# Kernel tuning notes

Hardware: AMD Instinct MI355X
Metric: run time of the kernel (lower is better)

## Reference

```python
import jax, jax.numpy as jnp
import numpy as np

N = 100000   # nodes
E = 1600000  # edges (avg degree 16)
IN = 24
HID = 128
OUT = 12


def setup_inputs() -> dict:
    key = jax.random.key(0)
    ks = jax.random.split(key, 16)
    s = 0.05
    return {
        "inputs": jax.random.normal(ks[0], (N, IN), jnp.float32),
        "src": jax.random.randint(ks[1], (E,), 0, N),
        "dst": jax.random.randint(ks[2], (E,), 0, N),
        "e_w": jax.random.uniform(ks[3], (E, 1), jnp.float32),
        "snorm_n": jax.random.uniform(ks[4], (N, 1), jnp.float32),
        "snorm_e": jax.random.uniform(ks[5], (E, 1), jnp.float32),
        "W_emb": jax.random.normal(ks[6], (IN, HID), jnp.float32) * s,
        "b_emb": jnp.zeros((HID,), jnp.float32),
        "W_self1": jax.random.normal(ks[7], (HID, HID), jnp.float32) * s,
        "W1": jax.random.normal(ks[8], (HID, HID), jnp.float32) * s,
        "b1": jnp.zeros((HID,), jnp.float32),
        "W_self2": jax.random.normal(ks[9], (HID, HID), jnp.float32) * s,
        "W2": jax.random.normal(ks[10], (HID, HID), jnp.float32) * s,
        "b2": jnp.zeros((HID,), jnp.float32),
        "W_fc": jax.random.normal(ks[11], (HID, OUT), jnp.float32) * s,
        "b_fc": jnp.zeros((OUT,), jnp.float32),
    }


def _degrees(src, dst):
    out_deg = jnp.clip(jnp.zeros((N,), jnp.float32).at[src].add(1.0), 1.0)
    in_deg = jnp.clip(jnp.zeros((N,), jnp.float32).at[dst].add(1.0), 1.0)
    return out_deg, in_deg


def _gcn_layer(h, src, dst, e_w, out_deg, in_deg, W_self, W, b):
    # self transform (no bias)
    h_s = h @ W_self
    # source-side symmetric norm, edge-weighted message, sum-aggregate at dst
    feat = h * (out_deg ** -0.5)[:, None]          # [N, H]
    m = feat[src] * e_w                            # [E, H]  u_mul_e
    agg = jax.ops.segment_sum(m, dst, num_segments=N)  # [N, H] sum reduce
    h2 = (agg @ W + b) * (in_deg ** -0.5)[:, None]
    return h_s + h2


def reference(inputs, src, dst, e_w, snorm_n, snorm_e,
              W_emb, b_emb, W_self1, W1, b1, W_self2, W2, b2, W_fc, b_fc):
    out_deg, in_deg = _degrees(src, dst)
    h = inputs @ W_emb + b_emb
    h = jax.nn.relu(_gcn_layer(h, src, dst, e_w, out_deg, in_deg, W_self1, W1, b1))
    h = jax.nn.relu(_gcn_layer(h, src, dst, e_w, out_deg, in_deg, W_self2, W2, b2))
    return h @ W_fc + b_fc
```

## Files before the change

### kernel.cpp

```cpp
#include <hip/hip_runtime.h>

#define NN 100000
#define EE 1600000
#define IN_F 24
#define HID 128
#define OUT_F 12
#define LBLK 128

#define NBKT 782
#define PA_BLKS 256
#define PA_EPB 6250

#define OW_BITS 13
#define OWIN 8192
#define OW_GRP 13
#define OW_CPY 48
#define OW_EPB 33334

#define RCAP 2560

#define EMB_B 2048
#define PREP_B 264
#define ONORM_B 196
#define K1_GRID (PA_BLKS + EMB_B + PREP_B + ONORM_B)

typedef unsigned char u8;
typedef unsigned short u16;
typedef unsigned int u32;
typedef unsigned long long u64;

using short8 = __attribute__((ext_vector_type(8))) short;
using f32x4  = __attribute__((ext_vector_type(4))) float;

__device__ __forceinline__ float bf2f(u16 h) {
  return __uint_as_float(((u32)h) << 16);
}
__device__ __forceinline__ u16 f2bf(float f) {
  u32 u = __float_as_uint(f);
  u32 r = (u + 0x7FFFu + ((u >> 16) & 1u)) >> 16;
  return (u16)r;
}
__device__ __forceinline__ float inv_sqrt_cnt(int c) {
  if (c < 1) c = 1;
  return 1.0f / sqrtf((float)c);
}

__global__ __launch_bounds__(256) void k_odeg(const int* __restrict__ src,
                                              u32* __restrict__ whist) {
  __shared__ u32 hist[OWIN / 2];
  int b = blockIdx.x, t = threadIdx.x;
  int g = b / OW_CPY, sb = b % OW_CPY;
  for (int i = t; i < OWIN / 2; i += 256) hist[i] = 0;
  __syncthreads();
  int e0 = sb * OW_EPB;
  int e1 = e0 + OW_EPB; if (e1 > EE) e1 = EE;
  for (int e = e0 + t; e < e1; e += 256) {
    int s = src[e];
    if ((s >> OW_BITS) == g) {
      int i = s & (OWIN - 1);
      atomicAdd(&hist[i >> 1], (i & 1) ? 0x10000u : 1u);
    }
  }
  __syncthreads();
  u32* out = whist + (size_t)b * (OWIN / 2);
  for (int i = t; i < OWIN / 2; i += 256) out[i] = hist[i];
}

__device__ __forceinline__ void emb_body(int eb, const float* __restrict__ inputs,
                                         const float* __restrict__ W_emb,
                                         const float* __restrict__ b_emb,
                                         u16* __restrict__ harr, float* smemW) {
  int t = threadIdx.x;
  float* Wls = smemW;
  float* bls = smemW + IN_F * HID;
  for (int i = t; i < IN_F * HID; i += 256) Wls[i] = W_emb[i];
  if (t < HID) bls[t] = b_emb[t];
  __syncthreads();
  int c = t & 127;
  int sub = t >> 7;
  for (int node = eb * 2 + sub; node < NN; node += EMB_B * 2) {
    const float* xr = inputs + (size_t)node * IN_F;
    float acc = bls[c];
    #pragma unroll
    for (int k = 0; k < IN_F; ++k) acc = fmaf(xr[k], Wls[k * HID + c], acc);
    harr[(size_t)node * HID + c] = f2bf(acc);
  }
}

__device__ __forceinline__ void prep_body(int pb,
    const float* __restrict__ Ws1, const float* __restrict__ W1m,
    const float* __restrict__ Ws2, const float* __restrict__ W2m,
    const float* __restrict__ Wfc,
    u16* __restrict__ WT1, u16* __restrict__ WT2, u16* __restrict__ WfcT) {
  int idx = pb * 256 + (int)threadIdx.x;
  if (idx < 65536) {
    int layer = idx >> 15;
    int rem = idx & 32767;
    int n = rem >> 8, k = rem & 255;
    const float* A = layer ? Ws2 : Ws1;
    const float* B = layer ? W2m : W1m;
    float v = (k < HID) ? A[(size_t)k * HID + n] : B[(size_t)(k - HID) * HID + n];
    (layer ? WT2 : WT1)[(size_t)n * 256 + k] = f2bf(v);
  } else if (idx < 65536 + 2048) {
    int j = idx - 65536;
    int n = j >> 7, k = j & 127;
    WfcT[(size_t)n * 128 + k] = f2bf(n < OUT_F ? Wfc[(size_t)k * OUT_F + n] : 0.f);
  }
}

__device__ __forceinline__ void onorm_body(int ob, const u32* __restrict__ whist,
                                           float* __restrict__ out_norm) {
  int i = ob * 256 + (int)threadIdx.x;
  if (i >= NN / 2) return;
  int n0 = 2 * i;
  int g = n0 >> OW_BITS;
  int pi = (n0 & (OWIN - 1)) >> 1;
  const u32* base = whist + (size_t)g * OW_CPY * (OWIN / 2) + pi;
  u32 s = 0;
  #pragma unroll 8
  for (int c = 0; c < OW_CPY; ++c) s += base[(size_t)c * (OWIN / 2)];
  out_norm[n0]     = inv_sqrt_cnt((int)(s & 0xFFFFu));
  out_norm[n0 + 1] = inv_sqrt_cnt((int)(s >> 16));
}

__global__ __launch_bounds__(256) void k1(
    const int* __restrict__ dst, u32* __restrict__ histgD,
    const float* __restrict__ inputs, const float* __restrict__ W_emb,
    const float* __restrict__ b_emb, u16* __restrict__ harr,
    const float* __restrict__ Ws1, const float* __restrict__ W1m,
    const float* __restrict__ Ws2, const float* __restrict__ W2m,
    const float* __restrict__ Wfc,
    u16* __restrict__ WT1, u16* __restrict__ WT2, u16* __restrict__ WfcT,
    const u32* __restrict__ whist, float* __restrict__ out_norm) {
  __shared__ __align__(16) char sm[13312];
  int b = blockIdx.x, t = threadIdx.x;
  if (b < PA_BLKS) {
    u32* histD = (u32*)sm;
    for (int i = t; i < 1024; i += 256) histD[i] = 0;
    __syncthreads();
    int e0 = b * PA_EPB;
    for (int e = e0 + t; e < e0 + PA_EPB; e += 256)
      atomicAdd(&histD[dst[e] >> 7], 1u);
    __syncthreads();
    for (int i = t; i < 1024; i += 256) histgD[(size_t)b * 1024 + i] = histD[i];
  } else if (b < PA_BLKS + EMB_B) {
    emb_body(b - PA_BLKS, inputs, W_emb, b_emb, harr, (float*)sm);
  } else if (b < PA_BLKS + EMB_B + PREP_B) {
    prep_body(b - PA_BLKS - EMB_B, Ws1, W1m, Ws2, W2m, Wfc, WT1, WT2, WfcT);
  } else {
    onorm_body(b - PA_BLKS - EMB_B - PREP_B, whist, out_norm);
  }
}

__global__ __launch_bounds__(256) void k_scan1(u32* __restrict__ histgD,
                                               u32* __restrict__ totalsD) {
  __shared__ u32 s[256];
  int k = blockIdx.x, t = threadIdx.x;
  u32 v = histgD[(size_t)t * 1024 + k];
  s[t] = v;
  __syncthreads();
  for (int off = 1; off < 256; off <<= 1) {
    u32 a = (t >= off) ? s[t - off] : 0;
    __syncthreads();
    s[t] += a;
    __syncthreads();
  }
  histgD[(size_t)t * 1024 + k] = s[t] - v;
  if (t == 255) totalsD[k] = s[255];
}

__global__ __launch_bounds__(1024) void k_scan2(const u32* __restrict__ totalsD,
                                                u32* __restrict__ estartD) {
  __shared__ u32 s[1024];
  int t = threadIdx.x;
  u32 v = (t < NBKT) ? totalsD[t] : 0;
  s[t] = v;
  __syncthreads();
  for (int off = 1; off < 1024; off <<= 1) {
    u32 a = (t >= off) ? s[t - off] : 0;
    __syncthreads();
    s[t] += a;
    __syncthreads();
  }
  if (t < NBKT) estartD[t] = s[t] - v;
  if (t == NBKT - 1) estartD[NBKT] = s[t];
}

__global__ __launch_bounds__(256) void k_passb(
    const int* __restrict__ src, const int* __restrict__ dst,
    const float* __restrict__ e_w,
    const u32* __restrict__ histgD, const u32* __restrict__ estartD,
    u64* __restrict__ ebuf) {
  __shared__ u32 cur[1024];
  int pb = blockIdx.x, t = threadIdx.x;
  for (int i = t; i < 1024; i += 256)
    cur[i] = ((i < NBKT) ? estartD[i] : 0u) + histgD[(size_t)pb * 1024 + i];
  __syncthreads();
  int e0 = pb * PA_EPB;
  for (int e = e0 + t; e < e0 + PA_EPB; e += 256) {
    int s = src[e], d = dst[e];
    u32 hi = (u32)s | (((u32)(d & 127)) << 17);
    u64 rec = ((u64)hi << 32) | (u64)__float_as_uint(e_w[e]);
    u32 pos = atomicAdd(&cur[d >> 7], 1u);
    ebuf[pos] = rec;
  }
}

__global__ __launch_bounds__(256) void k_reorder(
    u64* __restrict__ ebuf, const u32* __restrict__ estart,
    int* __restrict__ row_start, float* __restrict__ in_norm) {
  __shared__ u64 stage[RCAP];
  __shared__ u32 cnt[128], pfx[128], cur[128];
  int k = blockIdx.x, t = threadIdx.x;
  if (t < 128) cnt[t] = 0;
  __syncthreads();
  int e0 = (int)estart[k], e1 = (int)estart[k + 1];
  int n = e1 - e0; if (n > RCAP) n = RCAP;
  for (int i = t; i < n; i += 256) {
    u64 v = ebuf[e0 + i];
    stage[i] = v;
    atomicAdd(&cnt[(u32)(v >> 49) & 127], 1u);
  }
  __syncthreads();
  if (t < 128) pfx[t] = cnt[t];
  __syncthreads();
  for (int off = 1; off < 128; off <<= 1) {
    u32 v = (t < 128 && t >= off) ? pfx[t - off] : 0;
    __syncthreads();
    if (t < 128) pfx[t] += v;
    __syncthreads();
  }
  if (t < 128) {
    u32 start = (u32)e0 + pfx[t] - cnt[t];
    cur[t] = start;
    int node = k * 128 + t;
    if (node < NN) {
      row_start[node] = (int)start;
      in_norm[node] = inv_sqrt_cnt((int)cnt[t]);
    }
  }
  if (k == NBKT - 1 && t == 0) row_start[NN] = e1;
  __syncthreads();
  for (int i = t; i < n; i += 256) {
    u64 v = stage[i];
    u32 pos = atomicAdd(&cur[(u32)(v >> 49) & 127], 1u);
    ebuf[pos] = v;
  }
}

__global__ __launch_bounds__(256) void k_agg(const u16* __restrict__ harr,
                                             const int* __restrict__ row_start,
                                             const float* __restrict__ in_norm,
                                             const float* __restrict__ out_norm,
                                             const u64* __restrict__ ebuf,
                                             u16* __restrict__ aggr) {
  int t = threadIdx.x;
  int node = blockIdx.x * 8 + (t >> 5);
  if (node >= NN) return;
  int lane = t & 31;
  int s0 = row_start[node], s1 = row_start[node + 1];
  float ax = 0.f, ay = 0.f, az = 0.f, aw = 0.f;
  for (int i0 = s0; i0 < s1; i0 += 32) {
    u32 pk2 = 0;
    if (i0 + lane < s1) {
      u64 rec = ebuf[i0 + lane];
      u32 sv = (u32)(rec >> 32) & 0x1FFFF;
      float w = __uint_as_float((u32)rec) * out_norm[sv];
      pk2 = (((u32)f2bf(w)) << 17) | sv;
    }
    int m = s1 - i0; if (m > 32) m = 32;
    int j = 0;
    for (; j + 4 <= m; j += 4) {
      u32 p0 = __shfl(pk2, j,     32);
      u32 p1 = __shfl(pk2, j + 1, 32);
      u32 p2 = __shfl(pk2, j + 2, 32);
      u32 p3 = __shfl(pk2, j + 3, 32);
      ushort4 h0 = *(const ushort4*)(harr + (size_t)(p0 & 0x1FFFF) * HID + lane * 4);
      ushort4 h1 = *(const ushort4*)(harr + (size_t)(p1 & 0x1FFFF) * HID + lane * 4);
      ushort4 h2 = *(const ushort4*)(harr + (size_t)(p2 & 0x1FFFF) * HID + lane * 4);
      ushort4 h3 = *(const ushort4*)(harr + (size_t)(p3 & 0x1FFFF) * HID + lane * 4);
      float w0 = bf2f((u16)(p0 >> 17));
      float w1 = bf2f((u16)(p1 >> 17));
      float w2 = bf2f((u16)(p2 >> 17));
      float w3 = bf2f((u16)(p3 >> 17));
      ax = fmaf(w0, bf2f(h0.x), ax); ay = fmaf(w0, bf2f(h0.y), ay);
      az = fmaf(w0, bf2f(h0.z), az); aw = fmaf(w0, bf2f(h0.w), aw);
      ax = fmaf(w1, bf2f(h1.x), ax); ay = fmaf(w1, bf2f(h1.y), ay);
      az = fmaf(w1, bf2f(h1.z), az); aw = fmaf(w1, bf2f(h1.w), aw);
      ax = fmaf(w2, bf2f(h2.x), ax); ay = fmaf(w2, bf2f(h2.y), ay);
      az = fmaf(w2, bf2f(h2.z), az); aw = fmaf(w2, bf2f(h2.w), aw);
      ax = fmaf(w3, bf2f(h3.x), ax); ay = fmaf(w3, bf2f(h3.y), ay);
      az = fmaf(w3, bf2f(h3.z), az); aw = fmaf(w3, bf2f(h3.w), aw);
    }
    for (; j < m; ++j) {
      u32 p = __shfl(pk2, j, 32);
      float w = bf2f((u16)(p >> 17));
      ushort4 hv = *(const ushort4*)(harr + (size_t)(p & 0x1FFFF) * HID + lane * 4);
      ax = fmaf(w, bf2f(hv.x), ax); ay = fmaf(w, bf2f(hv.y), ay);
      az = fmaf(w, bf2f(hv.z), az); aw = fmaf(w, bf2f(hv.w), aw);
    }
  }
  float inn = in_norm[node];
  ushort4 r;
  r.x = f2bf(ax * inn); r.y = f2bf(ay * inn);
  r.z = f2bf(az * inn); r.w = f2bf(aw * inn);
  *(ushort4*)(aggr + (size_t)node * HID + lane * 4) = r;
}

template<int FC>
__global__ __launch_bounds__(512) void k_layer(u16* __restrict__ harr,
    const u16* __restrict__ aggr,
    const u16* __restrict__ WT, const float* __restrict__ bias,
    const float* __restrict__ in_norm,
    const u16* __restrict__ WfcT, const float* __restrict__ b_fc,
    float* __restrict__ out) {
  __shared__ char smem[135168];
  const int t = threadIdx.x;
  const int r0 = blockIdx.x * LBLK;

  #pragma unroll
  for (int i = 0; i < 4; ++i) {
    int boff = i * 8192 + t * 16;
    int row = boff >> 8, col = boff & 255;
    uint4 v = *(const uint4*)(harr + (size_t)(r0 + row) * HID + (col >> 1));
    *(uint4*)(smem + row * 512 + (col ^ ((row & 7) << 4))) = v;
  }
  #pragma unroll
  for (int i = 0; i < 4; ++i) {
    int boff = i * 8192 + t * 16;
    int row = boff >> 8, col = boff & 255;
    uint4 v = *(const uint4*)(aggr + (size_t)(r0 + row) * HID + (col >> 1));
    *(uint4*)(smem + row * 512 + (256 + (col ^ ((row & 7) << 4)))) = v;
  }
  #pragma unroll
  for (int i = 0; i < 8; ++i) {
    int boff = i * 8192 + t * 16;
    int row = boff >> 9, col = boff & 511;
    uint4 v = *(const uint4*)(WT + (size_t)row * 256 + (col >> 1));
    *(uint4*)(smem + 65536 + row * 512 + (col ^ ((row & 7) << 4))) = v;
  }
  if (FC && t < 256) {
    int row = t >> 4, col = (t & 15) * 16;
    uint4 v = *(const uint4*)(WfcT + (size_t)row * 128 + (col >> 1));
    *(uint4*)(smem + 131072 + row * 256 + (col ^ ((row & 7) << 4))) = v;
  }
  __syncthreads();

  const int lane = t & 63, w = t >> 6;
  const int l15 = lane & 15, lhi = lane >> 4;

  f32x4 acc[8];
  #pragma unroll
  for (int nf = 0; nf < 8; ++nf) acc[nf] = (f32x4){0.f, 0.f, 0.f, 0.f};

  const int arow = w * 16 + l15;
  const char* pa = smem + arow * 512;
  const int aswz = (arow & 7) << 4;
  #pragma unroll
  for (int ks = 0; ks < 8; ++ks) {
    int kb = ks * 64 + (lhi << 4);
    short8 a = *(const short8*)(pa + (kb ^ aswz));
    #pragma unroll
    for (int nf = 0; nf < 8; ++nf) {
      int brow = nf * 16 + l15;
      short8 bf = *(const short8*)(smem + 65536 + brow * 512 + (kb ^ ((brow & 7) << 4)));
      acc[nf] = __builtin_amdgcn_mfma_f32_16x16x32_bf16(a, bf, acc[nf], 0, 0, 0);
    }
  }

  float bcol[8];
  #pragma unroll
  for (int nf = 0; nf < 8; ++nf) bcol[nf] = bias[nf * 16 + l15];

  if (!FC) {
    #pragma unroll
    for (int r = 0; r < 4; ++r) {
      int grow = r0 + w * 16 + (lhi << 2) + r;
      if (grow < NN) {
        float inn = in_norm[grow];
        #pragma unroll
        for (int nf = 0; nf < 8; ++nf) {
          float v = acc[nf][r] + inn * bcol[nf];
          harr[(size_t)grow * HID + nf * 16 + l15] = f2bf(fmaxf(v, 0.f));
        }
      }
    }
  } else {
    __syncthreads();
    #pragma unroll
    for (int r = 0; r < 4; ++r) {
      int lrow = w * 16 + (lhi << 2) + r;
      int grow = r0 + lrow;
      float inn = (grow < NN) ? in_norm[grow] : 0.f;
      #pragma unroll
      for (int nf = 0; nf < 8; ++nf) {
        int col = nf * 16 + l15;
        float v = fmaxf(acc[nf][r] + inn * bcol[nf], 0.f);
        *(u16*)(smem + lrow * 256 + ((col * 2) ^ ((lrow & 7) << 4))) = f2bf(v);
      }
    }
    __syncthreads();
    f32x4 a2 = (f32x4){0.f, 0.f, 0.f, 0.f};
    const char* pa2 = smem + (w * 16 + l15) * 256;
    const int as2 = (l15 & 7) << 4;
    #pragma unroll
    for (int ks = 0; ks < 4; ++ks) {
      int kb = ks * 64 + (lhi << 4);
      short8 a = *(const short8*)(pa2 + (kb ^ as2));
      short8 bf = *(const short8*)(smem + 131072 + l15 * 256 + (kb ^ as2));
      a2 = __builtin_amdgcn_mfma_f32_16x16x32_bf16(a, bf, a2, 0, 0, 0);
    }
    if (l15 < OUT_F) {
      float bo = b_fc[l15];
      #pragma unroll
      for (int r = 0; r < 4; ++r) {
        int grow = r0 + w * 16 + (lhi << 2) + r;
        if (grow < NN) out[(size_t)grow * OUT_F + l15] = a2[r] + bo;
      }
    }
  }
}

extern "C" void kernel_launch(void* const* d_in, const int* in_sizes, int n_in,
                              void* d_out, int out_size, void* d_ws, size_t ws_size,
                              hipStream_t stream) {
  (void)in_sizes; (void)n_in; (void)out_size;
  const float* inputs  = (const float*)d_in[0];
  const int*   src     = (const int*)d_in[1];
  const int*   dst     = (const int*)d_in[2];
  const float* e_w     = (const float*)d_in[3];
  const float* W_emb   = (const float*)d_in[6];
  const float* b_emb   = (const float*)d_in[7];
  const float* W_self1 = (const float*)d_in[8];
  const float* W1      = (const float*)d_in[9];
  const float* b1      = (const float*)d_in[10];
  const float* W_self2 = (const float*)d_in[11];
  const float* W2      = (const float*)d_in[12];
  const float* b2      = (const float*)d_in[13];
  const float* W_fc    = (const float*)d_in[14];
  const float* b_fc    = (const float*)d_in[15];
  float* out = (float*)d_out;

  u32* histgD      = (u32*)d_ws;
  u32* totalsD     = histgD + (size_t)PA_BLKS * 1024;
  u32* estartD     = totalsD + 1024;
  float* out_norm  = (float*)(estartD + 1024);
  float* in_norm   = out_norm + NN;
  int* row_start   = (int*)(in_norm + NN);
  u64* ebuf        = (u64*)(row_start + NN + 4);
  u16* harr        = (u16*)(ebuf + EE);
  u16* aggr        = harr + (size_t)NN * HID;
  u16* WT1         = aggr + (size_t)NN * HID;
  u16* WT2         = WT1 + 32768;
  u16* WfcT        = WT2 + 32768;
  u32* whist       = (u32*)ebuf;

  const size_t NEED = (size_t)PA_BLKS * 1024 * 4 + 2048 * 4 + (size_t)(3 * NN + 4) * 4
                      + (size_t)EE * 8 + (size_t)NN * HID * 4 + (2 * 32768 + 2048) * 2;
  if (ws_size < NEED) return;

  hipLaunchKernelGGL(k_odeg, dim3(OW_GRP * OW_CPY), dim3(256), 0, stream, src, whist);
  hipLaunchKernelGGL(k1, dim3(K1_GRID), dim3(256), 0, stream,
                     dst, histgD, inputs, W_emb, b_emb, harr,
                     W_self1, W1, W_self2, W2, W_fc, WT1, WT2, WfcT,
                     whist, out_norm);
  hipLaunchKernelGGL(k_scan1, dim3(NBKT), dim3(256), 0, stream, histgD, totalsD);
  hipLaunchKernelGGL(k_scan2, dim3(1), dim3(1024), 0, stream, totalsD, estartD);
  hipLaunchKernelGGL(k_passb, dim3(PA_BLKS), dim3(256), 0, stream,
                     src, dst, e_w, histgD, estartD, ebuf);
  hipLaunchKernelGGL(k_reorder, dim3(NBKT), dim3(256), 0, stream,
                     ebuf, estartD, row_start, in_norm);
  hipLaunchKernelGGL(k_agg, dim3((NN + 7) / 8), dim3(256), 0, stream,
                     harr, row_start, in_norm, out_norm, ebuf, aggr);
  hipLaunchKernelGGL(k_layer<0>, dim3((NN + LBLK - 1) / LBLK), dim3(512), 0, stream,
                     harr, aggr, WT1, b1, in_norm, WfcT, b_fc, out);
  hipLaunchKernelGGL(k_agg, dim3((NN + 7) / 8), dim3(256), 0, stream,
                     harr, row_start, in_norm, out_norm, ebuf, aggr);
  hipLaunchKernelGGL(k_layer<1>, dim3((NN + LBLK - 1) / LBLK), dim3(512), 0, stream,
                     harr, aggr, WT2, b2, in_norm, WfcT, b_fc, out);
}
```

Measured before the change: 352.2 us.

## Precompute packed edge weights in reorder; load GEMM A-fragments directly to registers

The reorder pass now multiplies each edge weight by the source out-norm and packs it as bf16 together with the source index. Both aggregation passes can then read the packed word without the per-edge out_norm gather. Separately, the layer kernel loads h and aggr A-operands straight from global memory into register fragments instead of staging them in shared memory. This halves LDS use, which may allow more blocks per CU, at the cost of higher register pressure and less coalesced loads.

```diff
diff --git a/kernel.cpp b/kernel.cpp
--- a/kernel.cpp
+++ b/kernel.cpp
@@ -208,6 +208,7 @@
 
 __global__ __launch_bounds__(256) void k_reorder(
     u64* __restrict__ ebuf, const u32* __restrict__ estart,
+    const float* __restrict__ out_norm,
     int* __restrict__ row_start, float* __restrict__ in_norm) {
   __shared__ u64 stage[RCAP];
   __shared__ u32 cnt[128], pfx[128], cur[128];
@@ -243,15 +244,18 @@
   __syncthreads();
   for (int i = t; i < n; i += 256) {
     u64 v = stage[i];
-    u32 pos = atomicAdd(&cur[(u32)(v >> 49) & 127], 1u);
-    ebuf[pos] = v;
+    u32 hi = (u32)(v >> 32);
+    u32 sv = hi & 0x1FFFF;
+    float w = __uint_as_float((u32)v) * out_norm[sv];
+    u64 nv = ((u64)hi << 32) | (u64)((((u32)f2bf(w)) << 17) | sv);
+    u32 pos = atomicAdd(&cur[(hi >> 17) & 127], 1u);
+    ebuf[pos] = nv;
   }
 }
 
 __global__ __launch_bounds__(256) void k_agg(const u16* __restrict__ harr,
                                              const int* __restrict__ row_start,
                                              const float* __restrict__ in_norm,
-                                             const float* __restrict__ out_norm,
                                              const u64* __restrict__ ebuf,
                                              u16* __restrict__ aggr) {
   int t = threadIdx.x;
@@ -262,12 +266,7 @@
   float ax = 0.f, ay = 0.f, az = 0.f, aw = 0.f;
   for (int i0 = s0; i0 < s1; i0 += 32) {
     u32 pk2 = 0;
-    if (i0 + lane < s1) {
-      u64 rec = ebuf[i0 + lane];
-      u32 sv = (u32)(rec >> 32) & 0x1FFFF;
-      float w = __uint_as_float((u32)rec) * out_norm[sv];
-      pk2 = (((u32)f2bf(w)) << 17) | sv;
-    }
+    if (i0 + lane < s1) pk2 = (u32)ebuf[i0 + lane];
     int m = s1 - i0; if (m > 32) m = 32;
     int j = 0;
     for (; j + 4 <= m; j += 4) {
@@ -314,57 +313,52 @@
     const float* __restrict__ in_norm,
     const u16* __restrict__ WfcT, const float* __restrict__ b_fc,
     float* __restrict__ out) {
-  __shared__ char smem[135168];
+  __shared__ char smem[69632];
   const int t = threadIdx.x;
   const int r0 = blockIdx.x * LBLK;
 
-  #pragma unroll
-  for (int i = 0; i < 4; ++i) {
-    int boff = i * 8192 + t * 16;
-    int row = boff >> 8, col = boff & 255;
-    uint4 v = *(const uint4*)(harr + (size_t)(r0 + row) * HID + (col >> 1));
-    *(uint4*)(smem + row * 512 + (col ^ ((row & 7) << 4))) = v;
-  }
-  #pragma unroll
-  for (int i = 0; i < 4; ++i) {
-    int boff = i * 8192 + t * 16;
-    int row = boff >> 8, col = boff & 255;
-    uint4 v = *(const uint4*)(aggr + (size_t)(r0 + row) * HID + (col >> 1));
-    *(uint4*)(smem + row * 512 + (256 + (col ^ ((row & 7) << 4)))) = v;
-  }
   #pragma unroll
   for (int i = 0; i < 8; ++i) {
     int boff = i * 8192 + t * 16;
     int row = boff >> 9, col = boff & 511;
     uint4 v = *(const uint4*)(WT + (size_t)row * 256 + (col >> 1));
-    *(uint4*)(smem + 65536 + row * 512 + (col ^ ((row & 7) << 4))) = v;
+    *(uint4*)(smem + row * 512 + (col ^ ((row & 7) << 4))) = v;
   }
   if (FC && t < 256) {
     int row = t >> 4, col = (t & 15) * 16;
     uint4 v = *(const uint4*)(WfcT + (size_t)row * 128 + (col >> 1));
-    *(uint4*)(smem + 131072 + row * 256 + (col ^ ((row & 7) << 4))) = v;
-  }
-  __syncthreads();
+    *(uint4*)(smem + 65536 + row * 256 + (col ^ ((row & 7) << 4))) = v;
+  }
 
   const int lane = t & 63, w = t >> 6;
   const int l15 = lane & 15, lhi = lane >> 4;
+  const int arow = w * 16 + l15;
+
+  short8 af[8];
+  {
+    const u16* rh = harr + (size_t)(r0 + arow) * HID;
+    const u16* ra = aggr + (size_t)(r0 + arow) * HID;
+    #pragma unroll
+    for (int ks = 0; ks < 8; ++ks) {
+      int kb = ks * 64 + (lhi << 4);
+      const u16* p = (kb < 256) ? (rh + (kb >> 1)) : (ra + ((kb - 256) >> 1));
+      af[ks] = *(const short8*)p;
+    }
+  }
+  __syncthreads();
 
   f32x4 acc[8];
   #pragma unroll
   for (int nf = 0; nf < 8; ++nf) acc[nf] = (f32x4){0.f, 0.f, 0.f, 0.f};
 
-  const int arow = w * 16 + l15;
-  const char* pa = smem + arow * 512;
-  const int aswz = (arow & 7) << 4;
   #pragma unroll
   for (int ks = 0; ks < 8; ++ks) {
     int kb = ks * 64 + (lhi << 4);
-    short8 a = *(const short8*)(pa + (kb ^ aswz));
     #pragma unroll
     for (int nf = 0; nf < 8; ++nf) {
       int brow = nf * 16 + l15;
-      short8 bf = *(const short8*)(smem + 65536 + brow * 512 + (kb ^ ((brow & 7) << 4)));
-      acc[nf] = __builtin_amdgcn_mfma_f32_16x16x32_bf16(a, bf, acc[nf], 0, 0, 0);
+      short8 bf = *(const short8*)(smem + brow * 512 + (kb ^ ((brow & 7) << 4)));
+      acc[nf] = __builtin_amdgcn_mfma_f32_16x16x32_bf16(af[ks], bf, acc[nf], 0, 0, 0);
     }
   }
 
@@ -407,7 +401,7 @@
     for (int ks = 0; ks < 4; ++ks) {
       int kb = ks * 64 + (lhi << 4);
       short8 a = *(const short8*)(pa2 + (kb ^ as2));
-      short8 bf = *(const short8*)(smem + 131072 + l15 * 256 + (kb ^ as2));
+      short8 bf = *(const short8*)(smem + 65536 + l15 * 256 + (kb ^ as2));
       a2 = __builtin_amdgcn_mfma_f32_16x16x32_bf16(a, bf, a2, 0, 0, 0);
     }
     if (l15 < OUT_F) {
@@ -469,13 +463,13 @@
   hipLaunchKernelGGL(k_passb, dim3(PA_BLKS), dim3(256), 0, stream,
                      src, dst, e_w, histgD, estartD, ebuf);
   hipLaunchKernelGGL(k_reorder, dim3(NBKT), dim3(256), 0, stream,
-                     ebuf, estartD, row_start, in_norm);
+                     ebuf, estartD, out_norm, row_start, in_norm);
   hipLaunchKernelGGL(k_agg, dim3((NN + 7) / 8), dim3(256), 0, stream,
-                     harr, row_start, in_norm, out_norm, ebuf, aggr);
+                     harr, row_start, in_norm, ebuf, aggr);
   hipLaunchKernelGGL(k_layer<0>, dim3((NN + LBLK - 1) / LBLK), dim3(512), 0, stream,
                      harr, aggr, WT1, b1, in_norm, WfcT, b_fc, out);
   hipLaunchKernelGGL(k_agg, dim3((NN + 7) / 8), dim3(256), 0, stream,
-                     harr, row_start, in_norm, out_norm, ebuf, aggr);
+                     harr, row_start, in_norm, ebuf, aggr);
   hipLaunchKernelGGL(k_layer<1>, dim3((NN + LBLK - 1) / LBLK), dim3(512), 0, stream,
                      harr, aggr, WT2, b2, in_norm, WfcT, b_fc, out);
 }
```

New measurement: 334.9 us. 4.9% less time.
